# Kernel optimization log

Hardware: AMD Instinct MI355X
Metric: run time of the kernel (lower is better)

The kernel has to match this reference:

```python
import jax, jax.numpy as jnp
import numpy as np

B, N, D, H = 2, 2048, 1024, 16
DK = D // H


def setup_inputs() -> dict:
    key = jax.random.key(0)
    ks = jax.random.split(key, 12)
    s = D ** -0.5
    inp = {
        "query": jax.random.normal(ks[0], (B, N, D), jnp.float32),
        "key": jax.random.normal(ks[1], (B, N, D), jnp.float32),
        "value": jax.random.normal(ks[2], (B, N, D), jnp.float32),
        # causal mask: 1 = keep, 0 = masked (matches create_causal_mask)
        "mask": jnp.tril(jnp.ones((N, N), jnp.int32)),
        "Wq": jax.random.normal(ks[3], (D, D), jnp.float32) * s,
        "bq": jnp.zeros((D,), jnp.float32),
        "Wk": jax.random.normal(ks[4], (D, D), jnp.float32) * s,
        "bk": jnp.zeros((D,), jnp.float32),
        "Wv": jax.random.normal(ks[5], (D, D), jnp.float32) * s,
        "bv": jnp.zeros((D,), jnp.float32),
        "Wo": jax.random.normal(ks[6], (D, D), jnp.float32) * s,
        "bo": jnp.zeros((D,), jnp.float32),
    }
    return inp


def reference(query, key, value, mask, Wq, bq, Wk, bk, Wv, bv, Wo, bo):
    scale = DK ** -0.5
    # Linear projections (torch nn.Linear: x @ W.T + b), split into heads -> [B,H,N,DK]
    q = (query @ Wq.T + bq).reshape(B, N, H, DK).transpose(0, 2, 1, 3)
    k = (key @ Wk.T + bk).reshape(B, N, H, DK).transpose(0, 2, 1, 3)
    v = (value @ Wv.T + bv).reshape(B, N, H, DK).transpose(0, 2, 1, 3)
    scores = jnp.einsum("bhqd,bhkd->bhqk", q, k) * scale  # [B,H,N,N]
    scores = jnp.where(mask[None, None, :, :] == 0, jnp.float32(-1e9), scores)
    attn = jax.nn.softmax(scores, axis=-1)
    ctx = jnp.einsum("bhqk,bhkd->bhqd", attn, v)  # [B,H,N,DK]
    ctx = ctx.transpose(0, 2, 1, 3).reshape(B, N, D)
    return ctx @ Wo.T + bo
```

## Files before the change

kernel.cpp:

```cpp
#include <hip/hip_runtime.h>
#include <hip/hip_bf16.h>

typedef __attribute__((ext_vector_type(4))) float f32x4;
typedef __attribute__((ext_vector_type(8))) __bf16 bf16x8;
typedef __attribute__((ext_vector_type(8))) unsigned short u16x8;
typedef __attribute__((ext_vector_type(4))) unsigned short u16x4;
typedef __attribute__((ext_vector_type(2))) unsigned int u32x2;
typedef unsigned short u16;

#define DEV static __device__ __forceinline__

DEV u16 f2bf(float f){
  unsigned u = __builtin_bit_cast(unsigned, f);
  u += 0x7fff + ((u >> 16) & 1);
  return (u16)(u >> 16);
}

DEV f32x4 mfma16(bf16x8 a, bf16x8 b, f32x4 c){
  return __builtin_amdgcn_mfma_f32_16x16x32_bf16(a, b, c, 0, 0, 0);
}

DEV void gload16(const void* g, void* l){
  __builtin_amdgcn_global_load_lds((const __attribute__((address_space(1))) void*)g,
                                   (__attribute__((address_space(3))) void*)l,
                                   16, 0, 0);
}

DEV float fexp2(float x){
#if __has_builtin(__builtin_amdgcn_exp2f)
  return __builtin_amdgcn_exp2f(x);
#else
  float r; asm("v_exp_f32 %0, %1" : "=v"(r) : "v"(x)); return r;
#endif
}

#define SCL 0.18033688011f
#define THR 11.0f
#define PLD 72

__global__ __launch_bounds__(256) void cvt_k(
    const float* __restrict__ s0, const float* __restrict__ s1,
    const float* __restrict__ s2, const float* __restrict__ s3,
    const float* __restrict__ s4, const float* __restrict__ s5,
    const float* __restrict__ s6,
    u16* __restrict__ d0, u16* __restrict__ d1, u16* __restrict__ d2,
    u16* __restrict__ d3, u16* __restrict__ d4, u16* __restrict__ d5,
    u16* __restrict__ d6){
  const int y = blockIdx.y;
  const float* __restrict__ s = y==0?s0:y==1?s1:y==2?s2:y==3?s3:y==4?s4:y==5?s5:s6;
  u16* __restrict__ d         = y==0?d0:y==1?d1:y==2?d2:y==3?d3:y==4?d4:y==5?d5:d6;
  const int n8 = (y < 3) ? (4096*1024/8) : (1024*1024/8);
  for (int i = blockIdx.x*256 + threadIdx.x; i < n8; i += gridDim.x*256){
    f32x4 a = *(const f32x4*)&s[(size_t)i*8];
    f32x4 b = *(const f32x4*)&s[(size_t)i*8 + 4];
    u16x8 h;
    #pragma unroll
    for (int j = 0; j < 4; ++j){ h[j] = f2bf(a[j]); h[j+4] = f2bf(b[j]); }
    *(u16x8*)&d[(size_t)i*8] = h;
  }
}

__global__ __launch_bounds__(256) void gemm_bt(
    const u16* __restrict__ A0, const u16* __restrict__ A1, const u16* __restrict__ A2,
    const u16* __restrict__ B0, const u16* __restrict__ B1, const u16* __restrict__ B2,
    const float* __restrict__ e0, const float* __restrict__ e1, const float* __restrict__ e2,
    u16* __restrict__ C0, u16* __restrict__ C1, u16* __restrict__ C2){
  __shared__ u16 As[2][128*32];
  __shared__ u16 Bs[2][128*32];
  const int z = blockIdx.z;
  const u16* __restrict__ A    = z==0 ? A0 : z==1 ? A1 : A2;
  const u16* __restrict__ Bw   = z==0 ? B0 : z==1 ? B1 : B2;
  const float* __restrict__ bias = z==0 ? e0 : z==1 ? e1 : e2;
  u16* __restrict__ C          = z==0 ? C0 : z==1 ? C1 : C2;
  const bool vt = (z == 2);
  const float qs = (z == 0) ? SCL : 1.0f;

  const int tid  = threadIdx.x;
  const int lane = tid & 63, w = tid >> 6;
  const int wr = w >> 1, wc = w & 1;
  const int l16 = lane & 15, lhi = lane >> 4;
  const int bm = vt ? blockIdx.x : blockIdx.y;
  const int bn = vt ? blockIdx.y : blockIdx.x;

  const int srow = w*16 + (lane >> 2);
  const int scol = (lane & 3)*8;
  const u16* Asrc = A  + (size_t)(bm*128 + srow)*1024 + scol;
  const u16* Bsrc = Bw + (size_t)(bn*128 + srow)*1024 + scol;
  const int d0 = w*512;

  f32x4 acc[4][4] = {};

  gload16(Asrc,             &As[0][d0]);
  gload16(Asrc + 64*1024,   &As[0][d0 + 2048]);
  gload16(Bsrc,             &Bs[0][d0]);
  gload16(Bsrc + 64*1024,   &Bs[0][d0 + 2048]);
  __syncthreads();

  for (int t = 0; t < 32; ++t){
    const int cur = t & 1, nxt = cur ^ 1;
    if (t < 31){
      const int k1 = (t + 1)*32;
      gload16(Asrc + k1,           &As[nxt][d0]);
      gload16(Asrc + 64*1024 + k1, &As[nxt][d0 + 2048]);
      gload16(Bsrc + k1,           &Bs[nxt][d0]);
      gload16(Bsrc + 64*1024 + k1, &Bs[nxt][d0 + 2048]);
    }
    bf16x8 af[4], bfr[4];
    #pragma unroll
    for (int mi = 0; mi < 4; ++mi)
      af[mi] = *(const bf16x8*)&As[cur][(wr*64 + mi*16 + l16)*32 + lhi*8];
    #pragma unroll
    for (int nf = 0; nf < 4; ++nf)
      bfr[nf] = *(const bf16x8*)&Bs[cur][(wc*64 + nf*16 + l16)*32 + lhi*8];
    #pragma unroll
    for (int mi = 0; mi < 4; ++mi)
      #pragma unroll
      for (int nf = 0; nf < 4; ++nf)
        acc[mi][nf] = mfma16(af[mi], bfr[nf], acc[mi][nf]);
    __syncthreads();
  }

  #pragma unroll
  for (int mi = 0; mi < 4; ++mi){
    #pragma unroll
    for (int nf = 0; nf < 4; ++nf){
      int row0 = bm*128 + wr*64 + mi*16 + lhi*4;
      int col  = bn*128 + wc*64 + nf*16 + l16;
      float bc = bias[col];
      #pragma unroll
      for (int r = 0; r < 4; ++r){
        int row = row0 + r;
        float val = (acc[mi][nf][r] + (vt ? bias[row] : bc)) * qs;
        if (!vt){
          int b = row >> 11, n = row & 2047;
          int h = col >> 6,  dk = col & 63;
          C[(((size_t)(b*16 + h))*2048 + n)*64 + dk] = f2bf(val);
        } else {
          int h = row >> 6,  dk = row & 63;
          int b = col >> 11, n = col & 2047;
          C[(((size_t)(b*16 + h))*64 + dk)*2048 + n] = f2bf(val);
        }
      }
    }
  }
}

__global__ __launch_bounds__(256) void gemm_o64(const u16* __restrict__ A,
                                                const u16* __restrict__ Bw,
                                                const float* __restrict__ bias,
                                                float* __restrict__ C){
  __shared__ u16 As[2][64*32];
  __shared__ u16 Bs[2][128*32];
  const int tid  = threadIdx.x;
  const int lane = tid & 63, w = tid >> 6;
  const int wr = w >> 1, wc = w & 1;
  const int l16 = lane & 15, lhi = lane >> 4;
  const int bm = blockIdx.y, bn = blockIdx.x;

  const int srow = w*16 + (lane >> 2);
  const int scol = (lane & 3)*8;
  const u16* Asrc = A  + (size_t)(bm*64  + srow)*1024 + scol;
  const u16* Bsrc = Bw + (size_t)(bn*128 + srow)*1024 + scol;
  const int d0 = w*512;

  f32x4 acc[2][4] = {};

  gload16(Asrc,           &As[0][d0]);
  gload16(Bsrc,           &Bs[0][d0]);
  gload16(Bsrc + 64*1024, &Bs[0][d0 + 2048]);
  __syncthreads();

  for (int t = 0; t < 32; ++t){
    const int cur = t & 1, nxt = cur ^ 1;
    if (t < 31){
      const int k1 = (t + 1)*32;
      gload16(Asrc + k1,           &As[nxt][d0]);
      gload16(Bsrc + k1,           &Bs[nxt][d0]);
      gload16(Bsrc + 64*1024 + k1, &Bs[nxt][d0 + 2048]);
    }
    bf16x8 af[2], bfr[4];
    #pragma unroll
    for (int mi = 0; mi < 2; ++mi)
      af[mi] = *(const bf16x8*)&As[cur][(wr*32 + mi*16 + l16)*32 + lhi*8];
    #pragma unroll
    for (int nf = 0; nf < 4; ++nf)
      bfr[nf] = *(const bf16x8*)&Bs[cur][(wc*64 + nf*16 + l16)*32 + lhi*8];
    #pragma unroll
    for (int mi = 0; mi < 2; ++mi)
      #pragma unroll
      for (int nf = 0; nf < 4; ++nf)
        acc[mi][nf] = mfma16(af[mi], bfr[nf], acc[mi][nf]);
    __syncthreads();
  }

  #pragma unroll
  for (int mi = 0; mi < 2; ++mi){
    #pragma unroll
    for (int nf = 0; nf < 4; ++nf){
      int row0 = bm*64 + wr*32 + mi*16 + lhi*4;
      int col  = bn*128 + wc*64 + nf*16 + l16;
      float bv = bias[col];
      #pragma unroll
      for (int r = 0; r < 4; ++r)
        C[(size_t)(row0 + r)*1024 + col] = acc[mi][nf][r] + bv;
    }
  }
}

DEV void sm_tile(int t, int qt, int q_abs,
                 const u16* __restrict__ Ksb, u16* __restrict__ PsW,
                 bf16x8 bq0, bf16x8 bq1,
                 f32x4* ctx, float& m_r, float& l_r,
                 int l16, int lhi, int lane, int swz){
  f32x4 s4[4] = {};
  #pragma unroll
  for (int nf = 0; nf < 4; ++nf){
    bf16x8 ak0 = *(const bf16x8*)&Ksb[(nf*16 + l16)*64 + ((lhi*8) ^ swz)];
    bf16x8 ak1 = *(const bf16x8*)&Ksb[(nf*16 + l16)*64 + ((32 + lhi*8) ^ swz)];
    s4[nf] = mfma16(ak0, bq0, s4[nf]);
    s4[nf] = mfma16(ak1, bq1, s4[nf]);
  }

  if (t == qt){
    #pragma unroll
    for (int nf = 0; nf < 4; ++nf)
      #pragma unroll
      for (int r = 0; r < 4; ++r){
        int kc = t*64 + nf*16 + lhi*4 + r;
        if (kc > q_abs) s4[nf][r] = -1.0e30f;
      }
  }

  float mt = fmaxf(
      fmaxf(fmaxf(fmaxf(s4[0][0],s4[0][1]), fmaxf(s4[0][2],s4[0][3])),
            fmaxf(fmaxf(s4[1][0],s4[1][1]), fmaxf(s4[1][2],s4[1][3]))),
      fmaxf(fmaxf(fmaxf(s4[2][0],s4[2][1]), fmaxf(s4[2][2],s4[2][3])),
            fmaxf(fmaxf(s4[3][0],s4[3][1]), fmaxf(s4[3][2],s4[3][3]))));
  mt = fmaxf(mt, __shfl_xor(mt, 16));
  mt = fmaxf(mt, __shfl_xor(mt, 32));

  if (!__all(mt <= m_r + THR)){
    float mn = fmaxf(m_r, mt);
    float sf = fexp2(m_r - mn);
    m_r = mn;
    l_r *= sf;
    float sfb[4];
    #pragma unroll
    for (int r = 0; r < 4; ++r)
      sfb[r] = __shfl(sf, (lane >> 4)*4 + r);
    #pragma unroll
    for (int dkf = 0; dkf < 4; ++dkf)
      #pragma unroll
      for (int r = 0; r < 4; ++r)
        ctx[dkf][r] *= sfb[r];
  }

  float lt = 0.f;
  u16* prow = PsW + l16*PLD;
  #pragma unroll
  for (int nf = 0; nf < 4; ++nf){
    float p0 = fexp2(s4[nf][0] - m_r);
    float p1 = fexp2(s4[nf][1] - m_r);
    float p2 = fexp2(s4[nf][2] - m_r);
    float p3 = fexp2(s4[nf][3] - m_r);
    lt += (p0 + p1) + (p2 + p3);
    unsigned w0 = __builtin_amdgcn_perm(__builtin_bit_cast(unsigned, p1),
                                        __builtin_bit_cast(unsigned, p0), 0x07060302u);
    unsigned w1 = __builtin_amdgcn_perm(__builtin_bit_cast(unsigned, p3),
                                        __builtin_bit_cast(unsigned, p2), 0x07060302u);
    u32x2 wp = {w0, w1};
    *(u32x2*)&prow[nf*16 + lhi*4] = wp;
  }
  lt += __shfl_xor(lt, 16);
  lt += __shfl_xor(lt, 32);
  l_r += lt;
}

DEV void pv_tile(const u16* __restrict__ Vsb, const u16* __restrict__ PsW,
                 f32x4* ctx, int l16, int lhi, int swz){
  const u16* prow = PsW + l16*PLD;
  __builtin_amdgcn_s_setprio(1);
  #pragma unroll
  for (int ks = 0; ks < 2; ++ks){
    bf16x8 pa = *(const bf16x8*)&prow[ks*32 + lhi*8];
    #pragma unroll
    for (int dkf = 0; dkf < 4; ++dkf){
      bf16x8 vb = *(const bf16x8*)&Vsb[(dkf*16 + l16)*64 + ((ks*32 + lhi*8) ^ swz)];
      ctx[dkf] = mfma16(pa, vb, ctx[dkf]);
    }
  }
  __builtin_amdgcn_s_setprio(0);
}

__global__ __launch_bounds__(256) void attn_k(const u16* __restrict__ Q,
                                              const u16* __restrict__ K,
                                              const u16* __restrict__ Vt,
                                              u16* __restrict__ CTX){
  __shared__ u16 Ks[2][64*64];
  __shared__ u16 Vs[2][64*64];
  __shared__ u16 Ps[4][2][16*PLD];
  const int tid  = threadIdx.x;
  const int lane = tid & 63, w = tid >> 6;
  const int l16 = lane & 15, lhi = lane >> 4;
  const int f  = blockIdx.x;
  const int bh = f & 31;
  const int qt = 31 - (f >> 5);
  const size_t base = (size_t)bh * 2048 * 64;
  const u16* Qb = Q  + base;
  const u16* Kb = K  + base;
  const u16* Vb = Vt + base;
  const int b = bh >> 4, h = bh & 15;

  const int s0 = tid, s1 = tid + 256;
  const int r0 = s0 >> 3, c0 = ((s0 & 7) ^ (r0 & 7))*8;
  const int r1 = s1 >> 3, c1 = ((s1 & 7) ^ (r1 & 7))*8;
  const u16* Ksrc0 = Kb + r0*64 + c0;
  const u16* Ksrc1 = Kb + r1*64 + c1;
  const u16* Vsrc0 = Vb + (size_t)r0*2048 + c0;
  const u16* Vsrc1 = Vb + (size_t)r1*2048 + c1;
  const int swz = (l16 & 7)*8;

  const int q_abs = qt*64 + w*16 + l16;
  bf16x8 bq0 = *(const bf16x8*)&Qb[(size_t)q_abs*64 + lhi*8];
  bf16x8 bq1 = *(const bf16x8*)&Qb[(size_t)q_abs*64 + 32 + lhi*8];

  f32x4 ctx[4] = {};
  float m_r = -3.0e38f, l_r = 0.f;
  u16* Ps0 = &Ps[w][0][0];
  u16* Ps1 = &Ps[w][1][0];

  gload16(Ksrc0, &Ks[0][s0*8]);  gload16(Ksrc1, &Ks[0][s1*8]);
  gload16(Vsrc0, &Vs[0][s0*8]);  gload16(Vsrc1, &Vs[0][s1*8]);
  __syncthreads();

  const int nt = qt + 1;
  for (int t = 0; t < nt; ++t){
    const int pb = t & 1;
    u16* PsC = pb ? Ps1 : Ps0;
    u16* PsP = pb ? Ps0 : Ps1;
    if (t + 1 < nt){
      gload16(Ksrc0 + (t+1)*4096, &Ks[pb^1][s0*8]);
      gload16(Ksrc1 + (t+1)*4096, &Ks[pb^1][s1*8]);
    }
    sm_tile(t, qt, q_abs, Ks[pb], PsC, bq0, bq1, ctx, m_r, l_r, l16, lhi, lane, swz);
    if (t > 0)
      pv_tile(Vs[pb^1], PsP, ctx, l16, lhi, swz);
    __syncthreads();
    if (t + 1 < nt){
      gload16(Vsrc0 + (size_t)(t+1)*64, &Vs[pb^1][s0*8]);
      gload16(Vsrc1 + (size_t)(t+1)*64, &Vs[pb^1][s1*8]);
    }
  }
  pv_tile(Vs[(nt-1)&1], (nt-1)&1 ? Ps1 : Ps0, ctx, l16, lhi, swz);

  float lf[4];
  #pragma unroll
  for (int r = 0; r < 4; ++r)
    lf[r] = __shfl(l_r, (lane >> 4)*4 + r);
  #pragma unroll
  for (int dkf = 0; dkf < 4; ++dkf)
    #pragma unroll
    for (int r = 0; r < 4; ++r){
      int q = qt*64 + w*16 + lhi*4 + r;
      CTX[((size_t)(b*2048 + q))*1024 + h*64 + dkf*16 + l16] = f2bf(ctx[dkf][r] / lf[r]);
    }
}

extern "C" void kernel_launch(void* const* d_in, const int* in_sizes, int n_in,
                              void* d_out, int out_size, void* d_ws, size_t ws_size,
                              hipStream_t stream){
  const float* q  = (const float*)d_in[0];
  const float* k  = (const float*)d_in[1];
  const float* v  = (const float*)d_in[2];
  const float* Wq = (const float*)d_in[4];  const float* bq = (const float*)d_in[5];
  const float* Wk = (const float*)d_in[6];  const float* bk = (const float*)d_in[7];
  const float* Wv = (const float*)d_in[8];  const float* bv = (const float*)d_in[9];
  const float* Wo = (const float*)d_in[10]; const float* bo = (const float*)d_in[11];
  float* out = (float*)d_out;
  dim3 blk(256);

  u16* Wqb = (u16*)d_ws;
  u16* Wkb = Wqb + 1048576;
  u16* Wvb = Wkb + 1048576;
  u16* Wob = Wvb + 1048576;
  u16* Xqb = Wob + 1048576;
  u16* Xkb = Xqb + 4194304;
  u16* Xvb = Xkb + 4194304;
  u16* Qw  = Xvb + 4194304;
  u16* Kw  = Qw + 4194304;
  u16* Vw  = Kw + 4194304;
  u16* Cw  = Xqb;

  cvt_k<<<dim3(512, 7), blk, 0, stream>>>(q, k, v, Wq, Wk, Wv, Wo,
                                          Xqb, Xkb, Xvb, Wqb, Wkb, Wvb, Wob);
  gemm_bt<<<dim3(8, 32, 3), blk, 0, stream>>>(
      Xqb, Xkb, Wvb, Wqb, Wkb, Xvb, bq, bk, bv, Qw, Kw, Vw);
  attn_k<<<dim3(1024), blk, 0, stream>>>(Qw, Kw, Vw, Cw);
  gemm_o64<<<dim3(8, 64), blk, 0, stream>>>(Cw, Wob, bo, out);
}
```

Baseline: 131.1 us.

## Enlarge attention query tile, swizzle GEMM grid, drop GEMM double buffering

The attention kernel now uses 512 threads (8 waves) per block, covering 128 query rows, so each K/V tile loaded into LDS is shared by twice as many waves. Per-wave diagonal masking handles the two 64-row halves. The QKV GEMM moves to a 1D grid with a remapped block order meant to group blocks onto XCDs for better L2 reuse. Both GEMMs drop LDS double buffering in favour of single-buffered, sync-bracketed loads, which may expose load latency but lowers LDS use and could raise occupancy.

Result: faster. 120.5 us (-8.1%).

```diff
diff --git a/kernel.cpp b/kernel.cpp
--- a/kernel.cpp
+++ b/kernel.cpp
@@ -65,59 +65,58 @@
     const u16* __restrict__ B0, const u16* __restrict__ B1, const u16* __restrict__ B2,
     const float* __restrict__ e0, const float* __restrict__ e1, const float* __restrict__ e2,
     u16* __restrict__ C0, u16* __restrict__ C1, u16* __restrict__ C2){
-  __shared__ u16 As[2][128*32];
-  __shared__ u16 Bs[2][128*32];
-  const int z = blockIdx.z;
+  __shared__ u16 As[128*32];
+  __shared__ u16 Bs[128*32];
+
+  const int f = blockIdx.x;
+  const int xc = f & 7, g = f >> 3;
+  const int p  = xc*12 + (g >> 3);
+  const int bn8 = g & 7;
+  const int z = p >> 5, bm32 = p & 31;
+  const bool vt = (z == 2);
+  const int bm = vt ? bn8 : bm32;
+  const int bn = vt ? bm32 : bn8;
+
   const u16* __restrict__ A    = z==0 ? A0 : z==1 ? A1 : A2;
   const u16* __restrict__ Bw   = z==0 ? B0 : z==1 ? B1 : B2;
   const float* __restrict__ bias = z==0 ? e0 : z==1 ? e1 : e2;
   u16* __restrict__ C          = z==0 ? C0 : z==1 ? C1 : C2;
-  const bool vt = (z == 2);
   const float qs = (z == 0) ? SCL : 1.0f;
 
   const int tid  = threadIdx.x;
   const int lane = tid & 63, w = tid >> 6;
   const int wr = w >> 1, wc = w & 1;
   const int l16 = lane & 15, lhi = lane >> 4;
-  const int bm = vt ? blockIdx.x : blockIdx.y;
-  const int bn = vt ? blockIdx.y : blockIdx.x;
 
   const int srow = w*16 + (lane >> 2);
   const int scol = (lane & 3)*8;
   const u16* Asrc = A  + (size_t)(bm*128 + srow)*1024 + scol;
   const u16* Bsrc = Bw + (size_t)(bn*128 + srow)*1024 + scol;
-  const int d0 = w*512;
+  u16* Adst0 = As + w*512;
+  u16* Bdst0 = Bs + w*512;
 
   f32x4 acc[4][4] = {};
 
-  gload16(Asrc,             &As[0][d0]);
-  gload16(Asrc + 64*1024,   &As[0][d0 + 2048]);
-  gload16(Bsrc,             &Bs[0][d0]);
-  gload16(Bsrc + 64*1024,   &Bs[0][d0 + 2048]);
-  __syncthreads();
-
-  for (int t = 0; t < 32; ++t){
-    const int cur = t & 1, nxt = cur ^ 1;
-    if (t < 31){
-      const int k1 = (t + 1)*32;
-      gload16(Asrc + k1,           &As[nxt][d0]);
-      gload16(Asrc + 64*1024 + k1, &As[nxt][d0 + 2048]);
-      gload16(Bsrc + k1,           &Bs[nxt][d0]);
-      gload16(Bsrc + 64*1024 + k1, &Bs[nxt][d0 + 2048]);
-    }
+  for (int k0 = 0; k0 < 1024; k0 += 32){
+    __syncthreads();
+    gload16(Asrc + k0,             Adst0);
+    gload16(Asrc + 64*1024 + k0,   Adst0 + 2048);
+    gload16(Bsrc + k0,             Bdst0);
+    gload16(Bsrc + 64*1024 + k0,   Bdst0 + 2048);
+    __syncthreads();
+
     bf16x8 af[4], bfr[4];
     #pragma unroll
     for (int mi = 0; mi < 4; ++mi)
-      af[mi] = *(const bf16x8*)&As[cur][(wr*64 + mi*16 + l16)*32 + lhi*8];
+      af[mi] = *(const bf16x8*)&As[(wr*64 + mi*16 + l16)*32 + lhi*8];
     #pragma unroll
     for (int nf = 0; nf < 4; ++nf)
-      bfr[nf] = *(const bf16x8*)&Bs[cur][(wc*64 + nf*16 + l16)*32 + lhi*8];
+      bfr[nf] = *(const bf16x8*)&Bs[(wc*64 + nf*16 + l16)*32 + lhi*8];
     #pragma unroll
     for (int mi = 0; mi < 4; ++mi)
       #pragma unroll
       for (int nf = 0; nf < 4; ++nf)
         acc[mi][nf] = mfma16(af[mi], bfr[nf], acc[mi][nf]);
-    __syncthreads();
   }
 
   #pragma unroll
@@ -149,8 +148,8 @@
                                                 const u16* __restrict__ Bw,
                                                 const float* __restrict__ bias,
                                                 float* __restrict__ C){
-  __shared__ u16 As[2][64*32];
-  __shared__ u16 Bs[2][128*32];
+  __shared__ u16 As[64*32];
+  __shared__ u16 Bs[128*32];
   const int tid  = threadIdx.x;
   const int lane = tid & 63, w = tid >> 6;
   const int wr = w >> 1, wc = w & 1;
@@ -161,36 +160,30 @@
   const int scol = (lane & 3)*8;
   const u16* Asrc = A  + (size_t)(bm*64  + srow)*1024 + scol;
   const u16* Bsrc = Bw + (size_t)(bn*128 + srow)*1024 + scol;
-  const int d0 = w*512;
+  u16* Adst0 = As + w*512;
+  u16* Bdst0 = Bs + w*512;
 
   f32x4 acc[2][4] = {};
 
-  gload16(Asrc,           &As[0][d0]);
-  gload16(Bsrc,           &Bs[0][d0]);
-  gload16(Bsrc + 64*1024, &Bs[0][d0 + 2048]);
-  __syncthreads();
-
-  for (int t = 0; t < 32; ++t){
-    const int cur = t & 1, nxt = cur ^ 1;
-    if (t < 31){
-      const int k1 = (t + 1)*32;
-      gload16(Asrc + k1,           &As[nxt][d0]);
-      gload16(Bsrc + k1,           &Bs[nxt][d0]);
-      gload16(Bsrc + 64*1024 + k1, &Bs[nxt][d0 + 2048]);
-    }
+  for (int k0 = 0; k0 < 1024; k0 += 32){
+    __syncthreads();
+    gload16(Asrc + k0,             Adst0);
+    gload16(Bsrc + k0,             Bdst0);
+    gload16(Bsrc + 64*1024 + k0,   Bdst0 + 2048);
+    __syncthreads();
+
     bf16x8 af[2], bfr[4];
     #pragma unroll
     for (int mi = 0; mi < 2; ++mi)
-      af[mi] = *(const bf16x8*)&As[cur][(wr*32 + mi*16 + l16)*32 + lhi*8];
+      af[mi] = *(const bf16x8*)&As[(wr*32 + mi*16 + l16)*32 + lhi*8];
     #pragma unroll
     for (int nf = 0; nf < 4; ++nf)
-      bfr[nf] = *(const bf16x8*)&Bs[cur][(wc*64 + nf*16 + l16)*32 + lhi*8];
+      bfr[nf] = *(const bf16x8*)&Bs[(wc*64 + nf*16 + l16)*32 + lhi*8];
     #pragma unroll
     for (int mi = 0; mi < 2; ++mi)
       #pragma unroll
       for (int nf = 0; nf < 4; ++nf)
         acc[mi][nf] = mfma16(af[mi], bfr[nf], acc[mi][nf]);
-    __syncthreads();
   }
 
   #pragma unroll
@@ -207,7 +200,7 @@
   }
 }
 
-DEV void sm_tile(int t, int qt, int q_abs,
+DEV void sm_tile(int t, int tdiag, int q_abs,
                  const u16* __restrict__ Ksb, u16* __restrict__ PsW,
                  bf16x8 bq0, bf16x8 bq1,
                  f32x4* ctx, float& m_r, float& l_r,
@@ -221,7 +214,7 @@
     s4[nf] = mfma16(ak1, bq1, s4[nf]);
   }
 
-  if (t == qt){
+  if (t >= tdiag){
     #pragma unroll
     for (int nf = 0; nf < 4; ++nf)
       #pragma unroll
@@ -292,35 +285,33 @@
   __builtin_amdgcn_s_setprio(0);
 }
 
-__global__ __launch_bounds__(256) void attn_k(const u16* __restrict__ Q,
+__global__ __launch_bounds__(512) void attn_k(const u16* __restrict__ Q,
                                               const u16* __restrict__ K,
                                               const u16* __restrict__ Vt,
                                               u16* __restrict__ CTX){
   __shared__ u16 Ks[2][64*64];
   __shared__ u16 Vs[2][64*64];
-  __shared__ u16 Ps[4][2][16*PLD];
+  __shared__ u16 Ps[8][2][16*PLD];
   const int tid  = threadIdx.x;
   const int lane = tid & 63, w = tid >> 6;
   const int l16 = lane & 15, lhi = lane >> 4;
   const int f  = blockIdx.x;
   const int bh = f & 31;
-  const int qt = 31 - (f >> 5);
+  const int qt = 15 - (f >> 5);
   const size_t base = (size_t)bh * 2048 * 64;
   const u16* Qb = Q  + base;
   const u16* Kb = K  + base;
   const u16* Vb = Vt + base;
   const int b = bh >> 4, h = bh & 15;
 
-  const int s0 = tid, s1 = tid + 256;
+  const int s0 = tid;
   const int r0 = s0 >> 3, c0 = ((s0 & 7) ^ (r0 & 7))*8;
-  const int r1 = s1 >> 3, c1 = ((s1 & 7) ^ (r1 & 7))*8;
   const u16* Ksrc0 = Kb + r0*64 + c0;
-  const u16* Ksrc1 = Kb + r1*64 + c1;
   const u16* Vsrc0 = Vb + (size_t)r0*2048 + c0;
-  const u16* Vsrc1 = Vb + (size_t)r1*2048 + c1;
   const int swz = (l16 & 7)*8;
 
-  const int q_abs = qt*64 + w*16 + l16;
+  const int q_abs = qt*128 + w*16 + l16;
+  const int tdiag = 2*qt + (w >> 2);
   bf16x8 bq0 = *(const bf16x8*)&Qb[(size_t)q_abs*64 + lhi*8];
   bf16x8 bq1 = *(const bf16x8*)&Qb[(size_t)q_abs*64 + 32 + lhi*8];
 
@@ -329,27 +320,23 @@
   u16* Ps0 = &Ps[w][0][0];
   u16* Ps1 = &Ps[w][1][0];
 
-  gload16(Ksrc0, &Ks[0][s0*8]);  gload16(Ksrc1, &Ks[0][s1*8]);
-  gload16(Vsrc0, &Vs[0][s0*8]);  gload16(Vsrc1, &Vs[0][s1*8]);
+  gload16(Ksrc0, &Ks[0][s0*8]);
+  gload16(Vsrc0, &Vs[0][s0*8]);
   __syncthreads();
 
-  const int nt = qt + 1;
+  const int nt = 2*qt + 2;
   for (int t = 0; t < nt; ++t){
     const int pb = t & 1;
     u16* PsC = pb ? Ps1 : Ps0;
     u16* PsP = pb ? Ps0 : Ps1;
-    if (t + 1 < nt){
+    if (t + 1 < nt)
       gload16(Ksrc0 + (t+1)*4096, &Ks[pb^1][s0*8]);
-      gload16(Ksrc1 + (t+1)*4096, &Ks[pb^1][s1*8]);
-    }
-    sm_tile(t, qt, q_abs, Ks[pb], PsC, bq0, bq1, ctx, m_r, l_r, l16, lhi, lane, swz);
+    sm_tile(t, tdiag, q_abs, Ks[pb], PsC, bq0, bq1, ctx, m_r, l_r, l16, lhi, lane, swz);
     if (t > 0)
       pv_tile(Vs[pb^1], PsP, ctx, l16, lhi, swz);
     __syncthreads();
-    if (t + 1 < nt){
+    if (t + 1 < nt)
       gload16(Vsrc0 + (size_t)(t+1)*64, &Vs[pb^1][s0*8]);
-      gload16(Vsrc1 + (size_t)(t+1)*64, &Vs[pb^1][s1*8]);
-    }
   }
   pv_tile(Vs[(nt-1)&1], (nt-1)&1 ? Ps1 : Ps0, ctx, l16, lhi, swz);
 
@@ -361,7 +348,7 @@
   for (int dkf = 0; dkf < 4; ++dkf)
     #pragma unroll
     for (int r = 0; r < 4; ++r){
-      int q = qt*64 + w*16 + lhi*4 + r;
+      int q = qt*128 + w*16 + lhi*4 + r;
       CTX[((size_t)(b*2048 + q))*1024 + h*64 + dkf*16 + l16] = f2bf(ctx[dkf][r] / lf[r]);
     }
 }
@@ -377,7 +364,6 @@
   const float* Wv = (const float*)d_in[8];  const float* bv = (const float*)d_in[9];
   const float* Wo = (const float*)d_in[10]; const float* bo = (const float*)d_in[11];
   float* out = (float*)d_out;
-  dim3 blk(256);
 
   u16* Wqb = (u16*)d_ws;
   u16* Wkb = Wqb + 1048576;
@@ -391,10 +377,10 @@
   u16* Vw  = Kw + 4194304;
   u16* Cw  = Xqb;
 
-  cvt_k<<<dim3(512, 7), blk, 0, stream>>>(q, k, v, Wq, Wk, Wv, Wo,
-                                          Xqb, Xkb, Xvb, Wqb, Wkb, Wvb, Wob);
-  gemm_bt<<<dim3(8, 32, 3), blk, 0, stream>>>(
+  cvt_k<<<dim3(512, 7), dim3(256), 0, stream>>>(q, k, v, Wq, Wk, Wv, Wo,
+                                                Xqb, Xkb, Xvb, Wqb, Wkb, Wvb, Wob);
+  gemm_bt<<<dim3(768), dim3(256), 0, stream>>>(
       Xqb, Xkb, Wvb, Wqb, Wkb, Xvb, bq, bk, bv, Qw, Kw, Vw);
-  attn_k<<<dim3(1024), blk, 0, stream>>>(Qw, Kw, Vw, Cw);
-  gemm_o64<<<dim3(8, 64), blk, 0, stream>>>(Cw, Wob, bo, out);
-}
+  attn_k<<<dim3(512), dim3(512), 0, stream>>>(Qw, Kw, Vw, Cw);
+  gemm_o64<<<dim3(8, 64), dim3(256), 0, stream>>>(Cw, Wob, bo, out);
+}
```
